# Optimization experiments

Measured on AMD Instinct MI355X. Metric: run time of the kernel, lower is better.

The kernel has to match this reference:

```python
import jax, jax.numpy as jnp
import numpy as np

B, SEQ_LEN, PRED_LEN, LABEL_LEN, PERIOD, N_CH = 32, 2048, 1024, 512, 256, 256
K = SEQ_LEN // PERIOD   # seg_num_x = 8
L = PRED_LEN // PERIOD  # seg_num_y = 4
EPS = 1e-5


def setup_inputs() -> dict:
    key = jax.random.key(0)
    k1, k2, k3, k4, k5, k6, k7 = jax.random.split(key, 7)
    x_enc = jax.random.normal(k1, (B, SEQ_LEN, N_CH), jnp.float32)
    x_mark_enc = jax.random.normal(k2, (B, SEQ_LEN, 4), jnp.float32)
    x_dec = jax.random.normal(k3, (B, LABEL_LEN + PRED_LEN, N_CH), jnp.float32)
    x_mark_dec = jax.random.normal(k4, (B, LABEL_LEN + PRED_LEN, 4), jnp.float32)
    # base_model abstracted as a linear map on the time axis of a [B, PERIOD, N] segment.
    # Scaled ~1/sqrt(P) so repeated powers (up to K+L-1 = 11) stay numerically tame.
    W_base = jax.random.normal(k5, (PERIOD, PERIOD), jnp.float32) * (0.9 / np.sqrt(PERIOD))
    # new_encoders[j]: nn.Linear(seg_num_x, 1) -> weight row [K] + bias scalar per j.
    W_enc = jax.random.normal(k6, (L, K), jnp.float32) * (1.0 / np.sqrt(K))
    b_enc = jax.random.normal(k7, (L,), jnp.float32) * 0.01
    return {"x_enc": x_enc, "x_mark_enc": x_mark_enc, "x_dec": x_dec,
            "x_mark_dec": x_mark_dec, "W_base": W_base, "W_enc": W_enc, "b_enc": b_enc}


def reference(x_enc, x_mark_enc, x_dec, x_mark_dec, W_base, W_enc, b_enc):
    Bv, S, N = x_enc.shape
    # per-series normalization over time (means is .detach()'d in torch; fwd math identical)
    means = jnp.mean(x_enc, axis=1, keepdims=True)                  # [B,1,N]
    xc = x_enc - means
    stdev = jnp.sqrt(jnp.var(xc, axis=1, keepdims=True) + EPS)      # [B,1,N]
    xn = xc / stdev

    # split into K segments of length PERIOD: [K, B, P, N]
    segs = xn.reshape(Bv, K, PERIOD, N).transpose(1, 0, 2, 3)

    # x_res[l][k] = base_model applied (K - k + l) times to segment k.
    # base(x) = einsum('qp,bpn->bqn', W_base, x), so m applications = W_base^m.
    def step(c, _):
        nxt = W_base @ c
        return nxt, nxt
    _, rest = jax.lax.scan(step, W_base, None, length=K + L - 2)
    powers = jnp.concatenate([W_base[None], rest], axis=0)          # powers[i] = W^(i+1)

    exps = (K - jnp.arange(K))[None, :] + jnp.arange(L)[:, None]    # [L,K]
    Wlk = powers[exps - 1]                                          # [L,K,P,P]
    x_res = jnp.einsum('lkqp,kbpn->lkbqn', Wlk, segs)               # [L,K,B,P,N]

    # dec_out_part[l] = sum_k W_enc[l,k] * x_res[l][k] + b_enc[l] * ones
    dec = jnp.einsum('lk,lkbqn->lbqn', W_enc, x_res) + b_enc[:, None, None, None]
    dec = dec.transpose(1, 0, 2, 3).reshape(Bv, L * PERIOD, N)      # cat over time

    # de-normalize
    dec = dec * stdev[:, 0, :][:, None, :] + means[:, 0, :][:, None, :]
    return dec[:, -PRED_LEN:, :]
```

## Files before the change

### kernel.cpp

```cpp
#include <hip/hip_runtime.h>
#include <cstdint>
#include <cstddef>


typedef unsigned short ushort_t;
typedef unsigned int uint_t;
typedef __attribute__((ext_vector_type(8))) short bf16x8;
typedef __attribute__((ext_vector_type(16))) float f32x16;

__device__ __forceinline__ ushort_t f32_to_bf16(float f) {
    uint_t u = __float_as_uint(f);
    u += 0x7FFFu + ((u >> 16) & 1u);
    return (ushort_t)(u >> 16);
}
__device__ __forceinline__ float bf16_to_f32(ushort_t h) {
    return __uint_as_float((uint_t)h << 16);
}

struct PowOps { int sa[4]; int sb[4]; int sd[4]; };

__global__ void powmul(float* __restrict__ Pw, PowOps ops) {
    __shared__ float As[4 * 256];
    const int mat = blockIdx.x;
    const int r0  = blockIdx.y * 4;
    const int tid = threadIdx.x;
    const float* A  = Pw + (size_t)ops.sa[mat] * 65536;
    const float* Bm = Pw + (size_t)ops.sb[mat] * 65536;
    float* C        = Pw + (size_t)ops.sd[mat] * 65536;
#pragma unroll
    for (int i = 0; i < 4; ++i) As[i * 256 + tid] = A[(size_t)(r0 + i) * 256 + tid];
    __syncthreads();
    float a0 = 0.f, a1 = 0.f, a2 = 0.f, a3 = 0.f;
    for (int p = 0; p < 256; p += 8) {
        float bv[8];
#pragma unroll
        for (int u = 0; u < 8; ++u) bv[u] = Bm[(size_t)(p + u) * 256 + tid];
#pragma unroll
        for (int u = 0; u < 8; ++u) {
            a0 += As[0 * 256 + p + u] * bv[u];
            a1 += As[1 * 256 + p + u] * bv[u];
            a2 += As[2 * 256 + p + u] * bv[u];
            a3 += As[3 * 256 + p + u] * bv[u];
        }
    }
    C[(size_t)(r0 + 0) * 256 + tid] = a0;
    C[(size_t)(r0 + 1) * 256 + tid] = a1;
    C[(size_t)(r0 + 2) * 256 + tid] = a2;
    C[(size_t)(r0 + 3) * 256 + tid] = a3;
}

__global__ void buildA(const float* __restrict__ Pw, const float* __restrict__ Wenc,
                       ushort_t* __restrict__ Ah, float* __restrict__ rsA) {
    __shared__ float red[4];
    const int t = blockIdx.x;
    const int l = t >> 8, q = t & 255;
    const int c = threadIdx.x;
    float part = 0.f;
#pragma unroll
    for (int k = 0; k < 8; ++k) {
        const int m = 8 - k + l;
        const float val = Wenc[l * 8 + k] * Pw[(size_t)(m - 1) * 65536 + q * 256 + c];
        const ushort_t h = f32_to_bf16(val);
        Ah[(size_t)t * 2048 + k * 256 + c] = h;
        part += bf16_to_f32(h);
    }
#pragma unroll
    for (int off = 32; off > 0; off >>= 1) part += __shfl_xor(part, off);
    if ((c & 63) == 0) red[c >> 6] = part;
    __syncthreads();
    if (c == 0) rsA[t] = red[0] + red[1] + red[2] + red[3];
}

__global__ void transpose_stats(const float* __restrict__ x, ushort_t* __restrict__ Xt,
                                float* __restrict__ ps1, float* __restrict__ ps2) {
    __shared__ float lds[64 * 65];
    __shared__ float red1[16 * 64];
    __shared__ float red2[16 * 64];
    const int st = blockIdx.x;
    const int nt = blockIdx.y;
    const int b  = blockIdx.z;
    const int tid = threadIdx.x;
    const int c = tid & 15, r = tid >> 4;
    const int s0 = st * 64;
    float s1[4] = {0,0,0,0}, s2[4] = {0,0,0,0};
#pragma unroll
    for (int it = 0; it < 4; ++it) {
        const int ii = r + it * 16;
        const float4 v = *(const float4*)(x + ((size_t)b * 2048 + s0 + ii) * 256 + nt * 64 + c * 4);
        const float vv[4] = {v.x, v.y, v.z, v.w};
#pragma unroll
        for (int j = 0; j < 4; ++j) {
            lds[ii * 65 + c * 4 + j] = vv[j];
            s1[j] += vv[j]; s2[j] += vv[j] * vv[j];
        }
    }
#pragma unroll
    for (int j = 0; j < 4; ++j) { red1[r * 64 + c * 4 + j] = s1[j]; red2[r * 64 + c * 4 + j] = s2[j]; }
    __syncthreads();
    if (tid < 64) {
        float a = 0.f, q = 0.f;
#pragma unroll
        for (int rr = 0; rr < 16; ++rr) { a += red1[rr * 64 + tid]; q += red2[rr * 64 + tid]; }
        const size_t o = (size_t)st * 8192 + b * 256 + nt * 64 + tid;
        ps1[o] = a; ps2[o] = q;
    }
#pragma unroll
    for (int step = 0; step < 8; ++step) {
        const int npr = step * 8 + (tid >> 5);
        const int sp  = (tid & 31) * 2;
        const float f0 = lds[sp * 65 + npr];
        const float f1 = lds[(sp + 1) * 65 + npr];
        const uint_t packed = (uint_t)f32_to_bf16(f0) | ((uint_t)f32_to_bf16(f1) << 16);
        *(uint_t*)(Xt + ((size_t)b * 256 + nt * 64 + npr) * 2048 + s0 + sp) = packed;
    }
}

#define GLOAD_LDS16(gsrc, ldst) \
    __builtin_amdgcn_global_load_lds((const __attribute__((address_space(1))) void*)(gsrc), \
                                     (__attribute__((address_space(3))) void*)(ldst), 16, 0, 0)

__global__ __launch_bounds__(512, 1) void gemm_kernel(
    const ushort_t* __restrict__ Ah,
    const ushort_t* __restrict__ Xt,
    const float* __restrict__ ps1, const float* __restrict__ ps2,
    const float* __restrict__ rsA, const float* __restrict__ benc,
    float* __restrict__ out)
{
    __shared__ ushort_t sA[2][2][4096];
    __shared__ ushort_t sX[2][2][8192];

    const int flat = blockIdx.x;
    const int xcd  = flat & 7;
    const int j    = flat >> 3;
    const int bx   = xcd + ((j & 3) << 3);
    const int by   = j >> 2;
    const int l    = by >> 1;

    const int tid  = threadIdx.x;
    const int lane = tid & 63;
    const int w    = tid >> 6;
    const int wm   = w >> 2;
    const int wn   = w & 3;
    const int li   = lane & 31, lg = lane >> 5;

    const int mg_l = lane >> 3;
    const int rh   = (lane >> 2) & 1;
    const int kc   = (lane & 3) ^ (mg_l & 3);
    const ushort_t* aBase  = Ah + (size_t)(by * 128 + w * 16 + 2 * mg_l + rh) * 2048 + kc * 8;
    const ushort_t* xBase0 = Xt + (size_t)(bx * 256 + w * 32 + 2 * mg_l + rh) * 2048 + kc * 8;
    const ushort_t* xBase1 = xBase0 + (size_t)16 * 2048;

#define STAGE_H(bf_, kt_, h_) do { \
    const int ko_ = (kt_) * 64 + (h_) * 32; \
    GLOAD_LDS16(aBase  + ko_, &sA[bf_][h_][w * 512]); \
    GLOAD_LDS16(xBase0 + ko_, &sX[bf_][h_][w * 1024]); \
    GLOAD_LDS16(xBase1 + ko_, &sX[bf_][h_][w * 1024 + 512]); \
} while (0)

    f32x16 acc[2][2];
#pragma unroll
    for (int mm = 0; mm < 2; ++mm)
#pragma unroll
        for (int nn = 0; nn < 2; ++nn)
#pragma unroll
            for (int rr = 0; rr < 16; ++rr) acc[mm][nn][rr] = 0.0f;

#define PHASE(bf_, h_, STAGEOPS, VMNT) do { \
    const ushort_t* pa_ = &sA[bf_][h_][0]; \
    const ushort_t* px_ = &sX[bf_][h_][0]; \
    bf16x8 af[2][2], xf[2][2]; \
    _Pragma("unroll") \
    for (int s_ = 0; s_ < 2; ++s_) { \
        const int ch_ = (s_ * 2 + lg) ^ ((li >> 1) & 3); \
        _Pragma("unroll") \
        for (int mm_ = 0; mm_ < 2; ++mm_) \
            af[s_][mm_] = *(const bf16x8*)(pa_ + (wm * 32 + mm_ * 16 + (li >> 1)) * 64 + (li & 1) * 32 + ch_ * 8); \
        _Pragma("unroll") \
        for (int nn_ = 0; nn_ < 2; ++nn_) \
            xf[s_][nn_] = *(const bf16x8*)(px_ + (wn * 32 + nn_ * 16 + (li >> 1)) * 64 + (li & 1) * 32 + ch_ * 8); \
    } \
    STAGEOPS; \
    VMNT; \
    asm volatile("" ::: "memory"); \
    __builtin_amdgcn_s_barrier(); \
    __builtin_amdgcn_s_setprio(1); \
    _Pragma("unroll") \
    for (int s_ = 0; s_ < 2; ++s_) \
        _Pragma("unroll") \
        for (int mm_ = 0; mm_ < 2; ++mm_) \
            _Pragma("unroll") \
            for (int nn_ = 0; nn_ < 2; ++nn_) \
                acc[mm_][nn_] = __builtin_amdgcn_mfma_f32_32x32x16_bf16(af[s_][mm_], xf[s_][nn_], acc[mm_][nn_], 0, 0, 0); \
    __builtin_amdgcn_s_setprio(0); \
    asm volatile("" ::: "memory"); \
    __builtin_amdgcn_s_barrier(); \
    asm volatile("" ::: "memory"); \
} while (0)

    STAGE_H(0, 0, 0);
    STAGE_H(0, 0, 1);
    asm volatile("s_waitcnt vmcnt(3)" ::: "memory");
    __builtin_amdgcn_s_barrier();
    asm volatile("" ::: "memory");

#pragma unroll 1
    for (int kt = 0; kt < 31; ++kt) {
        const int bf = kt & 1;
        PHASE(bf, 0, STAGE_H(bf ^ 1, kt + 1, 0),
              asm volatile("s_waitcnt vmcnt(3)" ::: "memory"));
        PHASE(bf, 1, STAGE_H(bf ^ 1, kt + 1, 1),
              asm volatile("s_waitcnt vmcnt(3)" ::: "memory"));
    }
    PHASE(1, 0, , asm volatile("s_waitcnt vmcnt(0)" ::: "memory"));
    PHASE(1, 1, , );
#undef PHASE
#undef STAGE_H

    const float be = benc[l];
    float mn[2], sd[2];
#pragma unroll
    for (int nn = 0; nn < 2; ++nn) {
        const int colp = wn * 64 + nn * 32 + li;
        float s = 0.f, q = 0.f;
#pragma unroll
        for (int st = 0; st < 32; ++st) {
            s += ps1[(size_t)st * 8192 + bx * 256 + colp];
            q += ps2[(size_t)st * 8192 + bx * 256 + colp];
        }
        const float mean = s * (1.0f / 2048.0f);
        float var = q * (1.0f / 2048.0f) - mean * mean;
        var = fmaxf(var, 0.0f);
        mn[nn] = mean;
        sd[nn] = sqrtf(var + 1e-5f);
    }
#pragma unroll
    for (int mm = 0; mm < 2; ++mm)
#pragma unroll
        for (int nn = 0; nn < 2; ++nn) {
            const int colp = wn * 64 + nn * 32 + li;
            const float ben = be * sd[nn];
#pragma unroll
            for (int rr = 0; rr < 16; ++rr) {
                const int row = by * 128 + wm * 64 + mm * 32 + ((rr & 3) + 8 * (rr >> 2) + 4 * lg);
                out[((size_t)bx * 1024 + row) * 256 + colp] =
                    acc[mm][nn][rr] + mn[nn] * (1.0f - rsA[row]) + ben;
            }
        }
}

extern "C" void kernel_launch(void* const* d_in, const int* in_sizes, int n_in,
                              void* d_out, int out_size, void* d_ws, size_t ws_size,
                              hipStream_t stream) {
    (void)in_sizes; (void)n_in; (void)out_size; (void)ws_size;
    const float* x_enc  = (const float*)d_in[0];
    const float* W_base = (const float*)d_in[4];
    const float* W_enc  = (const float*)d_in[5];
    const float* b_enc  = (const float*)d_in[6];
    float* out = (float*)d_out;

    char* ws = (char*)d_ws;
    float*    wsP   = (float*)(ws);
    float*    wsRsA = (float*)(ws + 0x300000);
    float*    wsS1  = (float*)(ws + 0x310000);
    float*    wsS2  = (float*)(ws + 0x410000);
    ushort_t* wsAh  = (ushort_t*)(ws + 0x510000);
    ushort_t* wsXt  = (ushort_t*)(ws + 0x910000);

    hipMemcpyAsync(wsP, W_base, 256 * 256 * sizeof(float), hipMemcpyDeviceToDevice, stream);

    { PowOps o{{0, 0, 0, 0}, {0, 0, 0, 0}, {1, 0, 0, 0}};
      powmul<<<dim3(1, 64), 256, 0, stream>>>(wsP, o); }
    { PowOps o{{1, 1, 0, 0}, {0, 1, 0, 0}, {2, 3, 0, 0}};
      powmul<<<dim3(2, 64), 256, 0, stream>>>(wsP, o); }
    { PowOps o{{3, 3, 3, 3}, {0, 1, 2, 3}, {4, 5, 6, 7}};
      powmul<<<dim3(4, 64), 256, 0, stream>>>(wsP, o); }
    { PowOps o{{7, 7, 7, 0}, {0, 1, 2, 0}, {8, 9, 10, 0}};
      powmul<<<dim3(3, 64), 256, 0, stream>>>(wsP, o); }

    buildA<<<1024, 256, 0, stream>>>(wsP, W_enc, wsAh, wsRsA);
    transpose_stats<<<dim3(32, 4, 32), 256, 0, stream>>>(x_enc, wsXt, wsS1, wsS2);

    gemm_kernel<<<dim3(256), 512, 0, stream>>>(wsAh, wsXt, wsS1, wsS2,
                                               wsRsA, b_enc, out);
}
```

Measured before the change: 118.0 us.

## Fuse prep kernels, drop memcpy, retile GEMM to 128x128 with triple buffering

Removes the device-to-device copy of W_base by reading it directly in powmul, and merges buildA and transpose_stats into a single prep launch to cut launch overhead. The GEMM moves from 512-thread 128x256 tiles to 256-thread 128x128 tiles with two blocks per CU, 512 blocks total, and a three-stage LDS ring with one barrier per k-step. The intent is better occupancy and latency hiding, at the cost of more blocks re-reading A and a different output column mapping.

```diff
diff --git a/kernel.cpp b/kernel.cpp
--- a/kernel.cpp
+++ b/kernel.cpp
@@ -19,13 +19,13 @@
 
 struct PowOps { int sa[4]; int sb[4]; int sd[4]; };
 
-__global__ void powmul(float* __restrict__ Pw, PowOps ops) {
+__global__ void powmul(const float* __restrict__ Wb, float* __restrict__ Pw, PowOps ops) {
     __shared__ float As[4 * 256];
     const int mat = blockIdx.x;
     const int r0  = blockIdx.y * 4;
     const int tid = threadIdx.x;
-    const float* A  = Pw + (size_t)ops.sa[mat] * 65536;
-    const float* Bm = Pw + (size_t)ops.sb[mat] * 65536;
+    const float* A  = (ops.sa[mat] < 0) ? Wb : Pw + (size_t)ops.sa[mat] * 65536;
+    const float* Bm = (ops.sb[mat] < 0) ? Wb : Pw + (size_t)ops.sb[mat] * 65536;
     float* C        = Pw + (size_t)ops.sd[mat] * 65536;
 #pragma unroll
     for (int i = 0; i < 4; ++i) As[i * 256 + tid] = A[(size_t)(r0 + i) * 256 + tid];
@@ -49,69 +49,72 @@
     C[(size_t)(r0 + 3) * 256 + tid] = a3;
 }
 
-__global__ void buildA(const float* __restrict__ Pw, const float* __restrict__ Wenc,
-                       ushort_t* __restrict__ Ah, float* __restrict__ rsA) {
-    __shared__ float red[4];
-    const int t = blockIdx.x;
-    const int l = t >> 8, q = t & 255;
-    const int c = threadIdx.x;
-    float part = 0.f;
-#pragma unroll
-    for (int k = 0; k < 8; ++k) {
-        const int m = 8 - k + l;
-        const float val = Wenc[l * 8 + k] * Pw[(size_t)(m - 1) * 65536 + q * 256 + c];
-        const ushort_t h = f32_to_bf16(val);
-        Ah[(size_t)t * 2048 + k * 256 + c] = h;
-        part += bf16_to_f32(h);
-    }
-#pragma unroll
-    for (int off = 32; off > 0; off >>= 1) part += __shfl_xor(part, off);
-    if ((c & 63) == 0) red[c >> 6] = part;
-    __syncthreads();
-    if (c == 0) rsA[t] = red[0] + red[1] + red[2] + red[3];
-}
-
-__global__ void transpose_stats(const float* __restrict__ x, ushort_t* __restrict__ Xt,
-                                float* __restrict__ ps1, float* __restrict__ ps2) {
+__global__ void prep(const float* __restrict__ x, ushort_t* __restrict__ Xt,
+                     float* __restrict__ ps1, float* __restrict__ ps2,
+                     const float* __restrict__ Pw, const float* __restrict__ Wb,
+                     const float* __restrict__ Wenc,
+                     ushort_t* __restrict__ Ah, float* __restrict__ rsA) {
     __shared__ float lds[64 * 65];
     __shared__ float red1[16 * 64];
     __shared__ float red2[16 * 64];
-    const int st = blockIdx.x;
-    const int nt = blockIdx.y;
-    const int b  = blockIdx.z;
+    const int bid = blockIdx.x;
     const int tid = threadIdx.x;
-    const int c = tid & 15, r = tid >> 4;
-    const int s0 = st * 64;
-    float s1[4] = {0,0,0,0}, s2[4] = {0,0,0,0};
-#pragma unroll
-    for (int it = 0; it < 4; ++it) {
-        const int ii = r + it * 16;
-        const float4 v = *(const float4*)(x + ((size_t)b * 2048 + s0 + ii) * 256 + nt * 64 + c * 4);
-        const float vv[4] = {v.x, v.y, v.z, v.w};
-#pragma unroll
-        for (int j = 0; j < 4; ++j) {
-            lds[ii * 65 + c * 4 + j] = vv[j];
-            s1[j] += vv[j]; s2[j] += vv[j] * vv[j];
-        }
-    }
-#pragma unroll
-    for (int j = 0; j < 4; ++j) { red1[r * 64 + c * 4 + j] = s1[j]; red2[r * 64 + c * 4 + j] = s2[j]; }
-    __syncthreads();
-    if (tid < 64) {
-        float a = 0.f, q = 0.f;
-#pragma unroll
-        for (int rr = 0; rr < 16; ++rr) { a += red1[rr * 64 + tid]; q += red2[rr * 64 + tid]; }
-        const size_t o = (size_t)st * 8192 + b * 256 + nt * 64 + tid;
-        ps1[o] = a; ps2[o] = q;
-    }
-#pragma unroll
-    for (int step = 0; step < 8; ++step) {
-        const int npr = step * 8 + (tid >> 5);
-        const int sp  = (tid & 31) * 2;
-        const float f0 = lds[sp * 65 + npr];
-        const float f1 = lds[(sp + 1) * 65 + npr];
-        const uint_t packed = (uint_t)f32_to_bf16(f0) | ((uint_t)f32_to_bf16(f1) << 16);
-        *(uint_t*)(Xt + ((size_t)b * 256 + nt * 64 + npr) * 2048 + s0 + sp) = packed;
+    if (bid < 4096) {
+        const int st = bid & 31;
+        const int nt = (bid >> 5) & 3;
+        const int b  = bid >> 7;
+        const int c = tid & 15, r = tid >> 4;
+        const int s0 = st * 64;
+        float s1[4] = {0,0,0,0}, s2[4] = {0,0,0,0};
+#pragma unroll
+        for (int it = 0; it < 4; ++it) {
+            const int ii = r + it * 16;
+            const float4 v = *(const float4*)(x + ((size_t)b * 2048 + s0 + ii) * 256 + nt * 64 + c * 4);
+            const float vv[4] = {v.x, v.y, v.z, v.w};
+#pragma unroll
+            for (int jj = 0; jj < 4; ++jj) {
+                lds[ii * 65 + c * 4 + jj] = vv[jj];
+                s1[jj] += vv[jj]; s2[jj] += vv[jj] * vv[jj];
+            }
+        }
+#pragma unroll
+        for (int jj = 0; jj < 4; ++jj) { red1[r * 64 + c * 4 + jj] = s1[jj]; red2[r * 64 + c * 4 + jj] = s2[jj]; }
+        __syncthreads();
+        if (tid < 64) {
+            float a = 0.f, q = 0.f;
+#pragma unroll
+            for (int rr = 0; rr < 16; ++rr) { a += red1[rr * 64 + tid]; q += red2[rr * 64 + tid]; }
+            const size_t o = (size_t)st * 8192 + b * 256 + nt * 64 + tid;
+            ps1[o] = a; ps2[o] = q;
+        }
+#pragma unroll
+        for (int step = 0; step < 8; ++step) {
+            const int npr = step * 8 + (tid >> 5);
+            const int sp  = (tid & 31) * 2;
+            const float f0 = lds[sp * 65 + npr];
+            const float f1 = lds[(sp + 1) * 65 + npr];
+            const uint_t packed = (uint_t)f32_to_bf16(f0) | ((uint_t)f32_to_bf16(f1) << 16);
+            *(uint_t*)(Xt + ((size_t)b * 256 + nt * 64 + npr) * 2048 + s0 + sp) = packed;
+        }
+    } else {
+        const int t = bid - 4096;
+        const int l = t >> 8, q = t & 255;
+        const int c = tid;
+        float part = 0.f;
+#pragma unroll
+        for (int k = 0; k < 8; ++k) {
+            const int m = 8 - k + l;
+            const float* src = (m == 1) ? Wb : (Pw + (size_t)(m - 2) * 65536);
+            const float val = Wenc[l * 8 + k] * src[q * 256 + c];
+            const ushort_t h = f32_to_bf16(val);
+            Ah[(size_t)t * 2048 + k * 256 + c] = h;
+            part += bf16_to_f32(h);
+        }
+#pragma unroll
+        for (int off = 32; off > 0; off >>= 1) part += __shfl_xor(part, off);
+        if ((c & 63) == 0) red1[c >> 6] = part;
+        __syncthreads();
+        if (c == 0) rsA[t] = red1[0] + red1[1] + red1[2] + red1[3];
     }
 }
 
@@ -119,42 +122,45 @@
     __builtin_amdgcn_global_load_lds((const __attribute__((address_space(1))) void*)(gsrc), \
                                      (__attribute__((address_space(3))) void*)(ldst), 16, 0, 0)
 
-__global__ __launch_bounds__(512, 1) void gemm_kernel(
+__global__ __launch_bounds__(256, 2) void gemm_kernel(
     const ushort_t* __restrict__ Ah,
     const ushort_t* __restrict__ Xt,
     const float* __restrict__ ps1, const float* __restrict__ ps2,
     const float* __restrict__ rsA, const float* __restrict__ benc,
     float* __restrict__ out)
 {
-    __shared__ ushort_t sA[2][2][4096];
-    __shared__ ushort_t sX[2][2][8192];
+    __shared__ ushort_t sA[3][4096];
+    __shared__ ushort_t sX[3][4096];
 
     const int flat = blockIdx.x;
     const int xcd  = flat & 7;
     const int j    = flat >> 3;
-    const int bx   = xcd + ((j & 3) << 3);
-    const int by   = j >> 2;
+    const int bx   = xcd + ((j & 7) << 3);
+    const int by   = j >> 3;
     const int l    = by >> 1;
 
     const int tid  = threadIdx.x;
     const int lane = tid & 63;
     const int w    = tid >> 6;
-    const int wm   = w >> 2;
-    const int wn   = w & 3;
+    const int wm   = w >> 1, wn = w & 1;
     const int li   = lane & 31, lg = lane >> 5;
-
-    const int mg_l = lane >> 3;
-    const int rh   = (lane >> 2) & 1;
-    const int kc   = (lane & 3) ^ (mg_l & 3);
-    const ushort_t* aBase  = Ah + (size_t)(by * 128 + w * 16 + 2 * mg_l + rh) * 2048 + kc * 8;
-    const ushort_t* xBase0 = Xt + (size_t)(bx * 256 + w * 32 + 2 * mg_l + rh) * 2048 + kc * 8;
-    const ushort_t* xBase1 = xBase0 + (size_t)16 * 2048;
-
-#define STAGE_H(bf_, kt_, h_) do { \
-    const int ko_ = (kt_) * 64 + (h_) * 32; \
-    GLOAD_LDS16(aBase  + ko_, &sA[bf_][h_][w * 512]); \
-    GLOAD_LDS16(xBase0 + ko_, &sX[bf_][h_][w * 1024]); \
-    GLOAD_LDS16(xBase1 + ko_, &sX[bf_][h_][w * 1024 + 512]); \
+    const int lq3  = (li >> 1) & 3;
+
+    const int lrow = 2 * (lane >> 3) + ((lane >> 2) & 1);
+    const int kc   = (lane & 3) ^ ((lane >> 3) & 3);
+    const ushort_t* aBase0 = Ah + (size_t)(by * 128 + 16 * (2 * w + 0) + lrow) * 2048 + kc * 8;
+    const ushort_t* aBase1 = Ah + (size_t)(by * 128 + 16 * (2 * w + 1) + lrow) * 2048 + kc * 8;
+    const ushort_t* xBase0 = Xt + (size_t)(bx * 128 + 16 * (2 * w + 0) + lrow) * 2048 + kc * 8;
+    const ushort_t* xBase1 = Xt + (size_t)(bx * 128 + 16 * (2 * w + 1) + lrow) * 2048 + kc * 8;
+
+    ushort_t* sAf = &sA[0][0];
+    ushort_t* sXf = &sX[0][0];
+
+#define STAGE(dst_off, ko_) do { \
+    GLOAD_LDS16(aBase0 + (ko_), sAf + (dst_off) + (2 * w + 0) * 512); \
+    GLOAD_LDS16(aBase1 + (ko_), sAf + (dst_off) + (2 * w + 1) * 512); \
+    GLOAD_LDS16(xBase0 + (ko_), sXf + (dst_off) + (2 * w + 0) * 512); \
+    GLOAD_LDS16(xBase1 + (ko_), sXf + (dst_off) + (2 * w + 1) * 512); \
 } while (0)
 
     f32x16 acc[2][2];
@@ -165,67 +171,57 @@
 #pragma unroll
             for (int rr = 0; rr < 16; ++rr) acc[mm][nn][rr] = 0.0f;
 
-#define PHASE(bf_, h_, STAGEOPS, VMNT) do { \
-    const ushort_t* pa_ = &sA[bf_][h_][0]; \
-    const ushort_t* px_ = &sX[bf_][h_][0]; \
-    bf16x8 af[2][2], xf[2][2]; \
-    _Pragma("unroll") \
-    for (int s_ = 0; s_ < 2; ++s_) { \
-        const int ch_ = (s_ * 2 + lg) ^ ((li >> 1) & 3); \
-        _Pragma("unroll") \
-        for (int mm_ = 0; mm_ < 2; ++mm_) \
-            af[s_][mm_] = *(const bf16x8*)(pa_ + (wm * 32 + mm_ * 16 + (li >> 1)) * 64 + (li & 1) * 32 + ch_ * 8); \
-        _Pragma("unroll") \
-        for (int nn_ = 0; nn_ < 2; ++nn_) \
-            xf[s_][nn_] = *(const bf16x8*)(px_ + (wn * 32 + nn_ * 16 + (li >> 1)) * 64 + (li & 1) * 32 + ch_ * 8); \
-    } \
-    STAGEOPS; \
-    VMNT; \
-    asm volatile("" ::: "memory"); \
-    __builtin_amdgcn_s_barrier(); \
-    __builtin_amdgcn_s_setprio(1); \
-    _Pragma("unroll") \
-    for (int s_ = 0; s_ < 2; ++s_) \
-        _Pragma("unroll") \
-        for (int mm_ = 0; mm_ < 2; ++mm_) \
-            _Pragma("unroll") \
-            for (int nn_ = 0; nn_ < 2; ++nn_) \
-                acc[mm_][nn_] = __builtin_amdgcn_mfma_f32_32x32x16_bf16(af[s_][mm_], xf[s_][nn_], acc[mm_][nn_], 0, 0, 0); \
-    __builtin_amdgcn_s_setprio(0); \
-    asm volatile("" ::: "memory"); \
-    __builtin_amdgcn_s_barrier(); \
-    asm volatile("" ::: "memory"); \
-} while (0)
-
-    STAGE_H(0, 0, 0);
-    STAGE_H(0, 0, 1);
-    asm volatile("s_waitcnt vmcnt(3)" ::: "memory");
-    __builtin_amdgcn_s_barrier();
-    asm volatile("" ::: "memory");
-
+    STAGE(0, 0);
+    STAGE(4096, 32);
+
+    int cb = 0;
 #pragma unroll 1
-    for (int kt = 0; kt < 31; ++kt) {
-        const int bf = kt & 1;
-        PHASE(bf, 0, STAGE_H(bf ^ 1, kt + 1, 0),
-              asm volatile("s_waitcnt vmcnt(3)" ::: "memory"));
-        PHASE(bf, 1, STAGE_H(bf ^ 1, kt + 1, 1),
-              asm volatile("s_waitcnt vmcnt(3)" ::: "memory"));
-    }
-    PHASE(1, 0, , asm volatile("s_waitcnt vmcnt(0)" ::: "memory"));
-    PHASE(1, 1, , );
-#undef PHASE
-#undef STAGE_H
+    for (int kt = 0; kt < 64; ++kt) {
+        if (kt < 63) { asm volatile("s_waitcnt vmcnt(4)" ::: "memory"); }
+        else         { asm volatile("s_waitcnt vmcnt(0)" ::: "memory"); }
+        __builtin_amdgcn_s_barrier();
+        asm volatile("" ::: "memory");
+
+        const ushort_t* pa = sAf + cb * 4096;
+        const ushort_t* px = sXf + cb * 4096;
+        bf16x8 af[2][2], xf[2][2];
+#pragma unroll
+        for (int ks = 0; ks < 2; ++ks) {
+            const int sl = ((ks << 1) + lg) ^ lq3;
+            const int ro = (li >> 1) * 64 + (li & 1) * 32 + sl * 8;
+            af[ks][0] = *(const bf16x8*)(pa + wm * 2048 + ro);
+            af[ks][1] = *(const bf16x8*)(pa + wm * 2048 + 1024 + ro);
+            xf[ks][0] = *(const bf16x8*)(px + wn * 2048 + ro);
+            xf[ks][1] = *(const bf16x8*)(px + wn * 2048 + 1024 + ro);
+        }
+        if (kt < 62) {
+            const int sb_ = (cb >= 1) ? cb - 1 : 2;
+            STAGE(sb_ * 4096, (kt + 2) * 32);
+        }
+        __builtin_amdgcn_s_setprio(1);
+#pragma unroll
+        for (int ks = 0; ks < 2; ++ks) {
+            acc[0][0] = __builtin_amdgcn_mfma_f32_32x32x16_bf16(af[ks][0], xf[ks][0], acc[0][0], 0, 0, 0);
+            acc[0][1] = __builtin_amdgcn_mfma_f32_32x32x16_bf16(af[ks][0], xf[ks][1], acc[0][1], 0, 0, 0);
+            acc[1][0] = __builtin_amdgcn_mfma_f32_32x32x16_bf16(af[ks][1], xf[ks][0], acc[1][0], 0, 0, 0);
+            acc[1][1] = __builtin_amdgcn_mfma_f32_32x32x16_bf16(af[ks][1], xf[ks][1], acc[1][1], 0, 0, 0);
+        }
+        __builtin_amdgcn_s_setprio(0);
+        asm volatile("" ::: "memory");
+        cb = (cb == 2) ? 0 : cb + 1;
+    }
+#undef STAGE
 
     const float be = benc[l];
     float mn[2], sd[2];
 #pragma unroll
     for (int nn = 0; nn < 2; ++nn) {
-        const int colp = wn * 64 + nn * 32 + li;
+        const int col = bx * 128 + wn * 64 + nn * 32 + li;
         float s = 0.f, q = 0.f;
 #pragma unroll
         for (int st = 0; st < 32; ++st) {
-            s += ps1[(size_t)st * 8192 + bx * 256 + colp];
-            q += ps2[(size_t)st * 8192 + bx * 256 + colp];
+            s += ps1[(size_t)st * 8192 + col];
+            q += ps2[(size_t)st * 8192 + col];
         }
         const float mean = s * (1.0f / 2048.0f);
         float var = q * (1.0f / 2048.0f) - mean * mean;
@@ -237,12 +233,13 @@
     for (int mm = 0; mm < 2; ++mm)
 #pragma unroll
         for (int nn = 0; nn < 2; ++nn) {
-            const int colp = wn * 64 + nn * 32 + li;
+            const int col = bx * 128 + wn * 64 + nn * 32 + li;
+            const int bq = col >> 8, nq = col & 255;
             const float ben = be * sd[nn];
 #pragma unroll
             for (int rr = 0; rr < 16; ++rr) {
                 const int row = by * 128 + wm * 64 + mm * 32 + ((rr & 3) + 8 * (rr >> 2) + 4 * lg);
-                out[((size_t)bx * 1024 + row) * 256 + colp] =
+                out[((size_t)bq * 1024 + row) * 256 + nq] =
                     acc[mm][nn][rr] + mn[nn] * (1.0f - rsA[row]) + ben;
             }
         }
@@ -266,20 +263,17 @@
     ushort_t* wsAh  = (ushort_t*)(ws + 0x510000);
     ushort_t* wsXt  = (ushort_t*)(ws + 0x910000);
 
-    hipMemcpyAsync(wsP, W_base, 256 * 256 * sizeof(float), hipMemcpyDeviceToDevice, stream);
-
-    { PowOps o{{0, 0, 0, 0}, {0, 0, 0, 0}, {1, 0, 0, 0}};
-      powmul<<<dim3(1, 64), 256, 0, stream>>>(wsP, o); }
-    { PowOps o{{1, 1, 0, 0}, {0, 1, 0, 0}, {2, 3, 0, 0}};
-      powmul<<<dim3(2, 64), 256, 0, stream>>>(wsP, o); }
-    { PowOps o{{3, 3, 3, 3}, {0, 1, 2, 3}, {4, 5, 6, 7}};
-      powmul<<<dim3(4, 64), 256, 0, stream>>>(wsP, o); }
-    { PowOps o{{7, 7, 7, 0}, {0, 1, 2, 0}, {8, 9, 10, 0}};
-      powmul<<<dim3(3, 64), 256, 0, stream>>>(wsP, o); }
-
-    buildA<<<1024, 256, 0, stream>>>(wsP, W_enc, wsAh, wsRsA);
-    transpose_stats<<<dim3(32, 4, 32), 256, 0, stream>>>(x_enc, wsXt, wsS1, wsS2);
-
-    gemm_kernel<<<dim3(256), 512, 0, stream>>>(wsAh, wsXt, wsS1, wsS2,
-                                               wsRsA, b_enc, out);
-}
+    { PowOps o{{-1, 0, 0, 0}, {-1, 0, 0, 0}, {0, 0, 0, 0}};
+      powmul<<<dim3(1, 64), 256, 0, stream>>>(W_base, wsP, o); }
+    { PowOps o{{0, 0, 0, 0}, {-1, 0, 0, 0}, {1, 2, 0, 0}};
+      powmul<<<dim3(2, 64), 256, 0, stream>>>(W_base, wsP, o); }
+    { PowOps o{{2, 2, 2, 2}, {-1, 0, 1, 2}, {3, 4, 5, 6}};
+      powmul<<<dim3(4, 64), 256, 0, stream>>>(W_base, wsP, o); }
+    { PowOps o{{6, 6, 6, 0}, {-1, 0, 1, 0}, {7, 8, 9, 0}};
+      powmul<<<dim3(3, 64), 256, 0, stream>>>(W_base, wsP, o); }
+
+    prep<<<5120, 256, 0, stream>>>(x_enc, wsXt, wsS1, wsS2, wsP, W_base, W_enc,
+                                   wsAh, wsRsA);
+
+    gemm_kernel<<<512, 256, 0, stream>>>(wsAh, wsXt, wsS1, wsS2, wsRsA, b_enc, out);
+}
```

Result: faster. 106.8 us (-9.5%).
